# Performance work log

Hardware: AMD Instinct MI355X
Metric: run time of the kernel (lower is better)

The kernel has to match this reference:

```python
import jax, jax.numpy as jnp
import numpy as np

K = 7  # window_size from init


def setup_inputs() -> dict:
    key = jax.random.key(0)
    k1, k2, k3 = jax.random.split(key, 3)
    B, S, C, H, W = 2, 5, 256, 200, 200
    hidden = max(C // 16, 4)  # 16
    feats = jax.random.normal(k1, (B, S, C, H, W), dtype=jnp.float32)
    w1 = jax.random.normal(k2, (hidden, C), dtype=jnp.float32) * (1.0 / np.sqrt(C))
    b1 = jnp.zeros((hidden,), dtype=jnp.float32)
    w2 = jax.random.normal(k3, (1, hidden), dtype=jnp.float32) * (1.0 / np.sqrt(hidden))
    b2 = jnp.zeros((1,), dtype=jnp.float32)
    return {"feats": feats, "w1": w1, "b1": b1, "w2": w2, "b2": b2}


def reference(feats, w1, b1, w2, b2):
    B, S, C, H, W = feats.shape
    pad_h = (K - H % K) % K
    pad_w = (K - W % K) % K
    x = jnp.pad(feats, ((0, 0), (0, 0), (0, 0), (0, pad_h), (0, pad_w)))
    Hp, Wp = H + pad_h, W + pad_w
    Hb, Wb = Hp // K, Wp // K
    # windowed view, matching torch unfold(3,k,k).unfold(4,k,k): [B,S,C,Hb,Wb,k,k]
    xw = x.reshape(B, S, C, Hb, K, Wb, K).transpose(0, 1, 2, 3, 5, 4, 6)
    # per-window channel descriptor: mean over the k x k window
    g = xw.mean(axis=(-1, -2))                      # [B,S,C,Hb,Wb]
    g = g.transpose(0, 1, 3, 4, 2)                  # [B,S,Hb,Wb,C]
    h = jax.nn.relu(jnp.einsum('bshwc,dc->bshwd', g, w1) + b1)
    logits = jnp.einsum('bshwd,od->bshwo', h, w2) + b2
    logits = logits[..., 0]                         # [B,S,Hb,Wb]
    # NOTE: faithful to source: softmax over dim=-1 (Wb axis), not the slice axis
    weights = jax.nn.softmax(logits, axis=-1)       # [B,S,Hb,Wb]
    # weighted sum over slices
    fused = jnp.einsum('bschwij,bshw->bchwij', xw, weights)  # [B,C,Hb,Wb,k,k]
    # faithful reassembly: permute(0,1,4,2,5,3) -> [B,C,k,Hb,k,Wb], then reshape
    fused = fused.transpose(0, 1, 4, 2, 5, 3).reshape(B, C, Hp, Wp)
    return fused[:, :, :H, :W]
```

## Files before the change

### kernel.cpp

```cpp
#include <hip/hip_runtime.h>
#include <math.h>

constexpr int B = 2, S = 5, C = 256, H = 200, W = 200;
constexpr int KW = 7;
constexpr int HB = 29, WB = 29;
constexpr int HID = 16;
constexpr int NW = HB * WB;

__global__ __launch_bounds__(256) void k_winsum(const float* __restrict__ feats,
                                                float* __restrict__ gsum) {
    const int blk = blockIdx.x;
    const float* src = feats + (size_t)blk * (H * W);

    __shared__ float colg[HB * W];

    const int tid = (int)threadIdx.x;

    for (int q = tid; q < HB * (W / 4); q += 256) {
        int hb = q / (W / 4);
        int x4 = q - hb * (W / 4);
        int y0 = hb * KW;
        float4 a = make_float4(0.f, 0.f, 0.f, 0.f);
#pragma unroll
        for (int i = 0; i < KW; ++i) {
            int y = y0 + i;
            if (y < H) {
                float4 v = ((const float4*)(src + (size_t)y * W))[x4];
                a.x += v.x; a.y += v.y; a.z += v.z; a.w += v.w;
            }
        }
        ((float4*)(colg + hb * W))[x4] = a;
    }
    __syncthreads();

    float* dst = gsum + (size_t)blk * NW;
    for (int p = tid; p < NW; p += 256) {
        int hb = p / WB;
        int wb = p - hb * WB;
        int x0 = wb * KW;
        float s = 0.f;
#pragma unroll
        for (int j = 0; j < KW; ++j) {
            int x = x0 + j;
            if (x < W) s += colg[hb * W + x];
        }
        dst[p] = s;
    }
}

__global__ __launch_bounds__(256) void k_weights(const float* __restrict__ gsum,
                                                 const float* __restrict__ w1,
                                                 const float* __restrict__ b1,
                                                 const float* __restrict__ w2,
                                                 const float* __restrict__ b2,
                                                 float* __restrict__ weights) {
    int blk = blockIdx.x;
    int hb = blk % HB; blk /= HB;
    int s  = blk % S;
    int b  = blk / S;
    const int bs = b * S + s;

    __shared__ float w1s[HID * C];
    __shared__ float part[8 * HID * WB];
    __shared__ float lg[WB];

    const int tid = (int)threadIdx.x;
    for (int i = tid; i < HID * C; i += 256) w1s[i] = w1[i];
    __syncthreads();

    if (tid < 8 * WB) {
        const int cg = tid / WB;
        const int wb = tid - cg * WB;
        float acc[HID];
#pragma unroll
        for (int d = 0; d < HID; ++d) acc[d] = 0.f;
        const float* g = gsum + (size_t)bs * C * NW + hb * WB + wb;
        const int c0 = cg * (C / 8);
        for (int c = c0; c < c0 + C / 8; ++c) {
            float gc = g[(size_t)c * NW];
#pragma unroll
            for (int d = 0; d < HID; ++d) acc[d] += gc * w1s[d * C + c];
        }
#pragma unroll
        for (int d = 0; d < HID; ++d) part[(cg * HID + d) * WB + wb] = acc[d];
    }
    __syncthreads();

    if (tid < WB) {
        float logit = b2[0];
#pragma unroll
        for (int d = 0; d < HID; ++d) {
            float a = 0.f;
#pragma unroll
            for (int cg = 0; cg < 8; ++cg) a += part[(cg * HID + d) * WB + tid];
            float h = a * (1.0f / 49.0f) + b1[d];
            logit += fmaxf(h, 0.0f) * w2[d];
        }
        lg[tid] = logit;
    }
    __syncthreads();
    if (tid < WB) {
        float m = -INFINITY;
        for (int t = 0; t < WB; ++t) m = fmaxf(m, lg[t]);
        float sum = 0.f;
        for (int t = 0; t < WB; ++t) sum += expf(lg[t] - m);
        weights[(size_t)bs * NW + hb * WB + tid] = expf(lg[tid] - m) / sum;
    }
}

constexpr int RPB = 4;
__global__ __launch_bounds__(256) void k_fuse(const float* __restrict__ feats,
                                              const float* __restrict__ weights,
                                              float* __restrict__ out) {
    int blk = blockIdx.x;
    const int g = blk % (H / RPB); blk /= (H / RPB);
    const int c = blk % C;
    const int b = blk / C;
    const int y0 = g * RPB;

    __shared__ float buf[S][RPB][W];
    __shared__ float wsl[S][RPB][WB];

    const int tid = (int)threadIdx.x;
    const size_t plane = (size_t)H * W;
    const size_t sstride = (size_t)C * plane;
    const float* f0 = feats + ((size_t)b * S * C + c) * plane;

    for (int q = tid; q < S * RPB * (W / 4); q += 256) {
        int s  = q / (RPB * (W / 4));
        int r  = q - s * (RPB * (W / 4));
        int yy = r / (W / 4);
        int xq = r - yy * (W / 4);
        int y  = y0 + yy;
        int i  = y / HB;
        int hb = y - i * HB;
        int y_in = hb * KW + i;
        float4 v = make_float4(0.f, 0.f, 0.f, 0.f);
        if (y_in < H)
            v = ((const float4*)(f0 + (size_t)s * sstride + (size_t)y_in * W))[xq];
        ((float4*)&buf[s][yy][0])[xq] = v;
    }
    for (int q = tid; q < S * RPB * WB; q += 256) {
        int s  = q / (RPB * WB);
        int r  = q - s * (RPB * WB);
        int yy = r / WB;
        int wb = r - yy * WB;
        int hb = (y0 + yy) % HB;
        wsl[s][yy][wb] = weights[((size_t)(b * S + s) * HB + hb) * WB + wb];
    }
    __syncthreads();

    float* o = out + ((size_t)b * C + c) * plane + (size_t)y0 * W;
    for (int p = tid; p < RPB * W; p += 256) {
        int yy = p / W;
        int x  = p - yy * W;
        int j  = x / WB;
        int wb = x - j * WB;
        int x_in = wb * KW + j;
        float acc = 0.f;
        if (x_in < W) {
#pragma unroll
            for (int s = 0; s < S; ++s)
                acc += buf[s][yy][x_in] * wsl[s][yy][wb];
        }
        o[p] = acc;
    }
}

extern "C" void kernel_launch(void* const* d_in, const int* in_sizes, int n_in,
                              void* d_out, int out_size, void* d_ws, size_t ws_size,
                              hipStream_t stream) {
    const float* feats = (const float*)d_in[0];
    const float* w1    = (const float*)d_in[1];
    const float* b1    = (const float*)d_in[2];
    const float* w2    = (const float*)d_in[3];
    const float* b2    = (const float*)d_in[4];
    float* out = (float*)d_out;

    float* gsum    = (float*)d_ws;
    float* weights = gsum + (size_t)B * S * C * NW;

    hipLaunchKernelGGL(k_winsum, dim3(B * S * C), dim3(256), 0, stream, feats, gsum);
    hipLaunchKernelGGL(k_weights, dim3(B * S * HB), dim3(256), 0, stream,
                       gsum, w1, b1, w2, b2, weights);
    hipLaunchKernelGGL(k_fuse, dim3(B * C * (H / RPB)), dim3(256), 0, stream,
                       feats, weights, out);
}
```

Before: 194.8 us.

## Split pipeline per batch for cache reuse and vectorize fuse stores

Launches the winsum, weights and fuse kernels once per batch instead of once over all batches. The aim is for each batch's feature slab to stay resident in the large last-level cache between the window-sum pass and the fuse pass. The fuse kernel also writes four outputs per thread with float4 stores instead of scalar stores. In exchange there are more kernel launches, and the weights kernel runs with smaller grids.

```diff
diff --git a/kernel.cpp b/kernel.cpp
--- a/kernel.cpp
+++ b/kernel.cpp
@@ -8,8 +8,9 @@
 constexpr int NW = HB * WB;
 
 __global__ __launch_bounds__(256) void k_winsum(const float* __restrict__ feats,
-                                                float* __restrict__ gsum) {
-    const int blk = blockIdx.x;
+                                                float* __restrict__ gsum,
+                                                int b) {
+    const int blk = b * S * C + (int)blockIdx.x;
     const float* src = feats + (size_t)blk * (H * W);
 
     __shared__ float colg[HB * W];
@@ -53,11 +54,11 @@
                                                  const float* __restrict__ b1,
                                                  const float* __restrict__ w2,
                                                  const float* __restrict__ b2,
-                                                 float* __restrict__ weights) {
+                                                 float* __restrict__ weights,
+                                                 int b) {
     int blk = blockIdx.x;
-    int hb = blk % HB; blk /= HB;
-    int s  = blk % S;
-    int b  = blk / S;
+    int hb = blk % HB;
+    int s  = blk / HB;
     const int bs = b * S + s;
 
     __shared__ float w1s[HID * C];
@@ -111,11 +112,11 @@
 constexpr int RPB = 4;
 __global__ __launch_bounds__(256) void k_fuse(const float* __restrict__ feats,
                                               const float* __restrict__ weights,
-                                              float* __restrict__ out) {
+                                              float* __restrict__ out,
+                                              int b) {
     int blk = blockIdx.x;
-    const int g = blk % (H / RPB); blk /= (H / RPB);
-    const int c = blk % C;
-    const int b = blk / C;
+    const int g = blk % (H / RPB);
+    const int c = blk / (H / RPB);
     const int y0 = g * RPB;
 
     __shared__ float buf[S][RPB][W];
@@ -151,19 +152,26 @@
     __syncthreads();
 
     float* o = out + ((size_t)b * C + c) * plane + (size_t)y0 * W;
-    for (int p = tid; p < RPB * W; p += 256) {
-        int yy = p / W;
-        int x  = p - yy * W;
-        int j  = x / WB;
-        int wb = x - j * WB;
-        int x_in = wb * KW + j;
-        float acc = 0.f;
-        if (x_in < W) {
+    for (int p = tid; p < RPB * (W / 4); p += 256) {
+        int yy = p / (W / 4);
+        int x0 = (p - yy * (W / 4)) * 4;
+        float4 r;
+        float* rp = (float*)&r;
 #pragma unroll
-            for (int s = 0; s < S; ++s)
-                acc += buf[s][yy][x_in] * wsl[s][yy][wb];
+        for (int u = 0; u < 4; ++u) {
+            int x  = x0 + u;
+            int j  = x / WB;
+            int wb = x - j * WB;
+            int x_in = wb * KW + j;
+            float acc = 0.f;
+            if (x_in < W) {
+#pragma unroll
+                for (int s = 0; s < S; ++s)
+                    acc += buf[s][yy][x_in] * wsl[s][yy][wb];
+            }
+            rp[u] = acc;
         }
-        o[p] = acc;
+        ((float4*)(o + (size_t)yy * W))[x0 / 4] = r;
     }
 }
 
@@ -180,9 +188,12 @@
     float* gsum    = (float*)d_ws;
     float* weights = gsum + (size_t)B * S * C * NW;
 
-    hipLaunchKernelGGL(k_winsum, dim3(B * S * C), dim3(256), 0, stream, feats, gsum);
-    hipLaunchKernelGGL(k_weights, dim3(B * S * HB), dim3(256), 0, stream,
-                       gsum, w1, b1, w2, b2, weights);
-    hipLaunchKernelGGL(k_fuse, dim3(B * C * (H / RPB)), dim3(256), 0, stream,
-                       feats, weights, out);
+    for (int b = 0; b < B; ++b) {
+        hipLaunchKernelGGL(k_winsum, dim3(S * C), dim3(256), 0, stream,
+                           feats, gsum, b);
+        hipLaunchKernelGGL(k_weights, dim3(S * HB), dim3(256), 0, stream,
+                           gsum, w1, b1, w2, b2, weights, b);
+        hipLaunchKernelGGL(k_fuse, dim3(C * (H / RPB)), dim3(256), 0, stream,
+                           feats, weights, out, b);
+    }
 }
```

Result: slower. 204.8 us (+5.1%).
